# Kernel tuning notes

Hardware: AMD Instinct MI355X
Metric: run time of the kernel (lower is better)

## Reference

```python
import jax, jax.numpy as jnp
import numpy as np

K = 20  # neighbors


def knn_idx(x, k):
    # x: [B, C, N]; returns indices of k nearest neighbors (incl. self): [B, N, k]
    xx = jnp.sum(x * x, axis=1)                          # [B, N]
    inner = jnp.einsum('bcn,bcm->bnm', x, x)             # [B, N, N]
    pd = 2.0 * inner - xx[:, :, None] - xx[:, None, :]   # -squared distance
    _, idx = jax.lax.top_k(pd, k)                        # [B, N, k]
    return idx


def graph_feature(x, k):
    # x: [B, C, N] -> edge features [B, 2C, N, k]
    idx = knn_idx(x, k)                                  # [B, N, k]
    xt = jnp.swapaxes(x, 1, 2)                           # [B, N, C]
    nbr = jax.vmap(lambda f, i: f[i])(xt, idx)           # [B, N, k, C]
    ctr = xt[:, :, None, :]                              # [B, N, 1, C]
    feat = jnp.concatenate(
        [nbr - ctr, jnp.broadcast_to(ctr, nbr.shape)], axis=-1)  # [B, N, k, 2C]
    return jnp.transpose(feat, (0, 3, 1, 2))             # [B, 2C, N, k]


def blk2(x, w, s, t):
    # 1x1 Conv2d (no bias) + folded BN + LeakyReLU(0.2); x: [B, C, N, k]
    y = jnp.einsum('oc,bcnk->bonk', w, x)
    y = y * s[None, :, None, None] + t[None, :, None, None]
    return jax.nn.leaky_relu(y, 0.2)


def blk1(x, w, s, t):
    # 1x1 Conv1d (no bias) + folded BN + LeakyReLU(0.2); x: [B, C, N]
    y = jnp.einsum('oc,bcn->bon', w, x)
    y = y * s[None, :, None] + t[None, :, None]
    return jax.nn.leaky_relu(y, 0.2)


def setup_inputs() -> dict:
    key = jax.random.key(0)
    ks = jax.random.split(key, 32)
    inp = {'x': jax.random.normal(ks[0], (16, 2, 2048), jnp.float32)}
    wdims = [(64, 4), (64, 64), (64, 128), (64, 64), (64, 128),
             (1024, 192), (512, 1216), (256, 512), (1, 256)]
    for i, (o, c) in enumerate(wdims):
        inp[f'w{i+1}'] = jax.random.normal(ks[1 + i], (o, c), jnp.float32) * np.float32((2.0 / c) ** 0.5)
    bdims = [64, 64, 64, 64, 64, 1024, 512, 256]
    for i, d in enumerate(bdims):
        inp[f's{i+1}'] = jax.random.uniform(ks[10 + i], (d,), jnp.float32, 0.5, 1.5)
        inp[f't{i+1}'] = jax.random.normal(ks[18 + i], (d,), jnp.float32) * 0.1
    return inp


def reference(x, w1, w2, w3, w4, w5, w6, w7, w8, w9,
              s1, s2, s3, s4, s5, s6, s7, s8,
              t1, t2, t3, t4, t5, t6, t7, t8):
    B, _, N = x.shape
    h = graph_feature(x, K)                 # [B, 4, N, k]
    h = blk2(h, w1, s1, t1)
    h = blk2(h, w2, s2, t2)
    x1 = jnp.max(h, axis=-1)                # [B, 64, N]
    h = graph_feature(x1, K)                # [B, 128, N, k]
    h = blk2(h, w3, s3, t3)
    h = blk2(h, w4, s4, t4)
    x2 = jnp.max(h, axis=-1)                # [B, 64, N]
    h = graph_feature(x2, K)                # [B, 128, N, k]
    h = blk2(h, w5, s5, t5)
    x3 = jnp.max(h, axis=-1)                # [B, 64, N]
    cat = jnp.concatenate([x1, x2, x3], axis=1)   # [B, 192, N]
    e = blk1(cat, w6, s6, t6)               # [B, 1024, N]
    g = jnp.max(e, axis=-1, keepdims=True)  # global max [B, 1024, 1]
    g = jnp.broadcast_to(g, (B, g.shape[1], N))
    h = jnp.concatenate([g, x1, x2, x3], axis=1)  # [B, 1216, N]
    h = blk1(h, w7, s7, t7)
    h = blk1(h, w8, s8, t8)                 # dropout = identity (eval)
    y = jnp.einsum('oc,bcn->bon', w9, h)    # [B, 1, N]
    return jax.nn.sigmoid(y.reshape(B, -1))
```

## Files before the change

kernel.cpp:

```cpp
#include <hip/hip_runtime.h>
#include <math.h>

#define KNNK 20
#define BEFORE(v1, g1, v2, g2) (((v1) > (v2)) || ((v1) == (v2) && (g1) < (g2)))

typedef unsigned short u16;
typedef unsigned int u32;
typedef __attribute__((ext_vector_type(8))) short short8v;
typedef __attribute__((ext_vector_type(4))) float f32x4;

__device__ __forceinline__ float lrelu(float v) { return v >= 0.f ? v : 0.2f * v; }

__device__ __forceinline__ u16 f2bf(float v) {
    u32 u = __float_as_uint(v);
    u += 0x7fffu + ((u >> 16) & 1u);
    return (u16)(u >> 16);
}
__device__ __forceinline__ float bf2f(u16 h) { return __uint_as_float(((u32)h) << 16); }

__global__ __launch_bounds__(256) void xx_kernel(const float* __restrict__ f, long bstride, int C,
                                                 float* __restrict__ xx) {
    int i = blockIdx.x * 256 + threadIdx.x;
    int b = i >> 11, n = i & 2047;
    const float* fb = f + (long)b * bstride;
    float s = 0.f;
    for (int c = 0; c < C; ++c) { float v = fb[c * 2048 + n]; s = fmaf(v, v, s); }
    xx[i] = s;
}

__global__ __launch_bounds__(512, 4) void knn_kernel(const float* __restrict__ f, long bstride, int C,
                                                     const float* __restrict__ xx, int* __restrict__ idx_out) {
    __shared__ __align__(16) float lds[8 * 2048];
    int b = blockIdx.y;
    int n0 = blockIdx.x * 8;
    int t = threadIdx.x;
    const float* fb = f + (long)b * bstride;

    for (int e = t; e < C * 8; e += 512) {
        int c = e >> 3, j = e & 7;
        lds[e] = fb[c * 2048 + n0 + j];
    }
    __syncthreads();

    float acc[8][4];
#pragma unroll
    for (int i = 0; i < 8; ++i)
#pragma unroll
        for (int j = 0; j < 4; ++j) acc[i][j] = 0.f;
    int m0 = t * 4;
    for (int c = 0; c < C; ++c) {
        float4 b4 = *(const float4*)(fb + c * 2048 + m0);
        float bv[4] = {b4.x, b4.y, b4.z, b4.w};
        float4 a0 = *(const float4*)(lds + c * 8);
        float4 a1 = *(const float4*)(lds + c * 8 + 4);
        float av[8] = {a0.x, a0.y, a0.z, a0.w, a1.x, a1.y, a1.z, a1.w};
#pragma unroll
        for (int i = 0; i < 8; ++i)
#pragma unroll
            for (int j = 0; j < 4; ++j) acc[i][j] = fmaf(av[i], bv[j], acc[i][j]);
    }
    float xn[8];
#pragma unroll
    for (int i = 0; i < 8; ++i) xn[i] = xx[b * 2048 + n0 + i];
    float4 xm4 = *(const float4*)(xx + b * 2048 + m0);
    float xm[4] = {xm4.x, xm4.y, xm4.z, xm4.w};

    __syncthreads();
#pragma unroll
    for (int i = 0; i < 8; ++i) {
        float4 o;
        o.x = (2.f * acc[i][0] - xn[i]) - xm[0];
        o.y = (2.f * acc[i][1] - xn[i]) - xm[1];
        o.z = (2.f * acc[i][2] - xn[i]) - xm[2];
        o.w = (2.f * acc[i][3] - xn[i]) - xm[3];
        *(float4*)(lds + i * 2048 + m0) = o;
    }
    __syncthreads();

    int wave = t >> 6, lane = t & 63;
    const float* srow = lds + wave * 2048;
    float v[32];
#pragma unroll
    for (int j = 0; j < 32; ++j) v[j] = srow[lane + 64 * j];

    float b1 = -INFINITY, b2 = -INFINITY, b3 = -INFINITY;
    int j1 = 0, j2 = 0, j3 = 0;
#pragma unroll
    for (int j = 0; j < 32; ++j) {
        float vv = v[j];
        bool c1 = vv > b1;
        bool c2 = vv > b2;
        bool c3 = vv > b3;
        b3 = c2 ? b2 : (c3 ? vv : b3);
        j3 = c2 ? j2 : (c3 ? j : j3);
        b2 = c1 ? b1 : (c2 ? vv : b2);
        j2 = c1 ? j1 : (c2 ? j : j2);
        b1 = c1 ? vv : b1;
        j1 = c1 ? j : j1;
    }

    float av = b1, bv = b2;
    int ag = lane + (j1 << 6), bg = lane + (j2 << 6);
#pragma unroll
    for (int size = 2; size <= 128; size <<= 1) {
#pragma unroll
        for (int stride = size >> 1; stride >= 1; stride >>= 1) {
            if (stride == 64) {
                bool keep = BEFORE(av, ag, bv, bg);
                float tv = keep ? av : bv;
                int tg = keep ? ag : bg;
                bv = keep ? bv : av; bg = keep ? bg : ag;
                av = tv; ag = tg;
            } else {
                float oav = __shfl_xor(av, stride), obv = __shfl_xor(bv, stride);
                int oag = __shfl_xor(ag, stride), obg = __shfl_xor(bg, stride);
                bool low = (lane & stride) == 0;
                bool ascA = (lane & size) == 0;
                bool ascB = (((64 + lane) & size) == 0);
                bool fA = BEFORE(av, ag, oav, oag);
                bool fB = BEFORE(bv, bg, obv, obg);
                bool tA = (low == ascA) ? fA : !fA;
                bool tB = (low == ascB) ? fB : !fB;
                av = tA ? av : oav; ag = tA ? ag : oag;
                bv = tB ? bv : obv; bg = tB ? bg : obg;
            }
        }
    }
    float wv19 = __shfl(av, 19);
    int wg19 = __shfl(ag, 19);
    unsigned used = (1u << j1) | (1u << j2) | (1u << j3);
    float pv = b3;
    int pg = lane + (j3 << 6);
    while (__any(BEFORE(pv, pg, wv19, wg19))) {
        unsigned long long act = __ballot(BEFORE(pv, pg, wv19, wg19));
        int L = __ffsll(act) - 1;
        float cv = __shfl(pv, L);
        int cg2 = __shfl(pg, L);
        unsigned long long cfb = __ballot(lane < 20 && BEFORE(cv, cg2, av, ag));
        int p = 20 - __popcll(cfb);
        float upv = __shfl_up(av, 1);
        int upg = __shfl_up(ag, 1);
        if (lane < 20) {
            if (lane > p) { av = upv; ag = upg; }
            else if (lane == p) { av = cv; ag = cg2; }
        }
        if (lane == L) {
            float nb = -INFINITY;
            int nj = 0;
#pragma unroll
            for (int j = 0; j < 32; ++j) {
                float vvv = ((used >> j) & 1u) ? -INFINITY : v[j];
                if (vvv > nb) { nb = vvv; nj = j; }
            }
            used |= 1u << nj;
            pv = nb;
            pg = lane + (nj << 6);
        }
        wv19 = __shfl(av, 19);
        wg19 = __shfl(ag, 19);
    }
    int* orow = idx_out + ((long)b * 2048 + n0 + wave) * KNNK;
    if (lane < KNNK) orow[lane] = ag;
}

__global__ __launch_bounds__(256) void pq_kernel(const float* __restrict__ f, long bstride, int C,
                                                 const float* __restrict__ W, float* __restrict__ P,
                                                 float* __restrict__ Q) {
    __shared__ __align__(16) float wa[64 * 64];
    __shared__ __align__(16) float wq[64 * 64];
    __shared__ __align__(16) float X[64 * 64];
    int b = blockIdx.y, n0 = blockIdx.x * 64, t = threadIdx.x;
    const float* fb = f + (long)b * bstride;
    for (int e = t; e < C * 64; e += 256) {
        int k = e >> 6, c = e & 63;
        float a = W[c * 2 * C + k];
        float bv = W[c * 2 * C + C + k];
        wa[k * 64 + c] = a;
        wq[k * 64 + c] = bv - a;
    }
    for (int e = t; e < C * 64; e += 256) {
        int k = e >> 6, j = e & 63;
        X[e] = fb[k * 2048 + n0 + j];
    }
    __syncthreads();
    int cg = t >> 4, ng = t & 15;
    float accP[4][4] = {}, accQ[4][4] = {};
    for (int k = 0; k < C; ++k) {
        float4 a4 = *(const float4*)(wa + k * 64 + cg * 4);
        float4 q4 = *(const float4*)(wq + k * 64 + cg * 4);
        float4 x4 = *(const float4*)(X + k * 64 + ng * 4);
        float av[4] = {a4.x, a4.y, a4.z, a4.w};
        float qv[4] = {q4.x, q4.y, q4.z, q4.w};
        float xv[4] = {x4.x, x4.y, x4.z, x4.w};
#pragma unroll
        for (int i = 0; i < 4; ++i)
#pragma unroll
            for (int j = 0; j < 4; ++j) {
                accP[i][j] = fmaf(av[i], xv[j], accP[i][j]);
                accQ[i][j] = fmaf(qv[i], xv[j], accQ[i][j]);
            }
    }
#pragma unroll
    for (int j = 0; j < 4; ++j) {
        long n = n0 + ng * 4 + j;
        float4 pv = {accP[0][j], accP[1][j], accP[2][j], accP[3][j]};
        float4 qv = {accQ[0][j], accQ[1][j], accQ[2][j], accQ[3][j]};
        *(float4*)(P + ((long)b * 2048 + n) * 64 + cg * 4) = pv;
        *(float4*)(Q + ((long)b * 2048 + n) * 64 + cg * 4) = qv;
    }
}

__global__ __launch_bounds__(256) void edge2_kernel(
    const float* __restrict__ P, const float* __restrict__ Q, const int* __restrict__ idx,
    const float* __restrict__ W2, const float* __restrict__ sa, const float* __restrict__ ta,
    const float* __restrict__ sb, const float* __restrict__ tb, float* __restrict__ out, int cofs) {
    __shared__ __align__(16) float h1[64 * 164];
    __shared__ __align__(16) float w2l[64 * 64];
    __shared__ int idxl[160];
    int b = blockIdx.y, n0 = blockIdx.x * 8, t = threadIdx.x;
    if (t < 160) idxl[t] = idx[((long)b * 2048 + n0) * KNNK + t];
    for (int e = t; e < 4096; e += 256) { int co = e >> 6, ci = e & 63; w2l[ci * 64 + co] = W2[e]; }
    __syncthreads();
    for (int it = t; it < 2560; it += 256) {
        int col = it % 160, cg = it / 160;
        int p = col / 20;
        int j = idxl[col];
        int n = n0 + p;
        float4 pv = *(const float4*)(P + ((long)b * 2048 + j) * 64 + cg * 4);
        float4 qv = *(const float4*)(Q + ((long)b * 2048 + n) * 64 + cg * 4);
        float4 sv = *(const float4*)(sa + cg * 4);
        float4 tv = *(const float4*)(ta + cg * 4);
        h1[(cg * 4 + 0) * 164 + col] = lrelu(fmaf(sv.x, pv.x + qv.x, tv.x));
        h1[(cg * 4 + 1) * 164 + col] = lrelu(fmaf(sv.y, pv.y + qv.y, tv.y));
        h1[(cg * 4 + 2) * 164 + col] = lrelu(fmaf(sv.z, pv.z + qv.z, tv.z));
        h1[(cg * 4 + 3) * 164 + col] = lrelu(fmaf(sv.w, pv.w + qv.w, tv.w));
    }
    __syncthreads();
    int p = t & 7, co2 = t >> 3, c0 = co2 * 2;
    float acc0[20], acc1[20];
#pragma unroll
    for (int q = 0; q < 20; ++q) { acc0[q] = 0.f; acc1[q] = 0.f; }
#pragma unroll 4
    for (int k = 0; k < 64; ++k) {
        float2 w = *(const float2*)(w2l + k * 64 + c0);
        const float* hr = h1 + k * 164 + p * 20;
#pragma unroll
        for (int q = 0; q < 5; ++q) {
            float4 h4 = *(const float4*)(hr + q * 4);
            acc0[q * 4 + 0] = fmaf(w.x, h4.x, acc0[q * 4 + 0]);
            acc0[q * 4 + 1] = fmaf(w.x, h4.y, acc0[q * 4 + 1]);
            acc0[q * 4 + 2] = fmaf(w.x, h4.z, acc0[q * 4 + 2]);
            acc0[q * 4 + 3] = fmaf(w.x, h4.w, acc0[q * 4 + 3]);
            acc1[q * 4 + 0] = fmaf(w.y, h4.x, acc1[q * 4 + 0]);
            acc1[q * 4 + 1] = fmaf(w.y, h4.y, acc1[q * 4 + 1]);
            acc1[q * 4 + 2] = fmaf(w.y, h4.z, acc1[q * 4 + 2]);
            acc1[q * 4 + 3] = fmaf(w.y, h4.w, acc1[q * 4 + 3]);
        }
    }
    float s0 = sb[c0], t0v = tb[c0], s1 = sb[c0 + 1], t1v = tb[c0 + 1];
    float m0 = -INFINITY, m1 = -INFINITY;
#pragma unroll
    for (int q = 0; q < 20; ++q) {
        m0 = fmaxf(m0, lrelu(fmaf(s0, acc0[q], t0v)));
        m1 = fmaxf(m1, lrelu(fmaf(s1, acc1[q], t1v)));
    }
    out[(long)b * (192 * 2048) + (long)(cofs + c0) * 2048 + n0 + p] = m0;
    out[(long)b * (192 * 2048) + (long)(cofs + c0 + 1) * 2048 + n0 + p] = m1;
}

__global__ __launch_bounds__(256) void edge1_kernel(const float* __restrict__ P, const float* __restrict__ Q,
                                                    const int* __restrict__ idx, const float* __restrict__ s,
                                                    const float* __restrict__ tt, float* __restrict__ out,
                                                    int cofs) {
    __shared__ int idxl[80];
    int b = blockIdx.y, n0 = blockIdx.x * 4, t = threadIdx.x;
    int c = t & 63, p = t >> 6;
    if (t < 80) idxl[t] = idx[((long)b * 2048 + n0) * KNNK + t];
    __syncthreads();
    float qv = Q[((long)b * 2048 + n0 + p) * 64 + c];
    float sc = s[c], tc = tt[c];
    float m = -INFINITY;
    for (int kk = 0; kk < KNNK; ++kk) {
        int j = idxl[p * KNNK + kk];
        float v = P[((long)b * 2048 + j) * 64 + c];
        m = fmaxf(m, lrelu(fmaf(sc, v + qv, tc)));
    }
    out[(long)b * (192 * 2048) + (long)(cofs + c) * 2048 + n0 + p] = m;
}

__global__ __launch_bounds__(256) void gemm_kernel(
    const float* __restrict__ W, int ldw, int Kdim, const float* __restrict__ X, long xbstride,
    const float* __restrict__ s, const float* __restrict__ tvec, const float* __restrict__ bias, int M,
    float* __restrict__ out, long obstride, float* __restrict__ maxout) {
    __shared__ __align__(16) float wl[32 * 68];
    __shared__ __align__(16) float xl[32 * 132];
    int b = blockIdx.z, ct = blockIdx.x * 64, nt = blockIdx.y * 128, t = threadIdx.x;
    const float* Xb = X + (long)b * xbstride;
    int cg = t >> 4, ng = t & 15;
    float acc[4][8];
#pragma unroll
    for (int i = 0; i < 4; ++i)
#pragma unroll
        for (int j = 0; j < 8; ++j) acc[i][j] = 0.f;
    for (int k0 = 0; k0 < Kdim; k0 += 32) {
        __syncthreads();
        for (int e = t; e < 2048; e += 256) {
            int c = e >> 5, k = e & 31;
            wl[k * 68 + c] = W[(long)(ct + c) * ldw + k0 + k];
        }
        for (int e = t; e < 4096; e += 256) {
            int k = e >> 7, j = e & 127;
            xl[k * 132 + j] = Xb[(long)(k0 + k) * 2048 + nt + j];
        }
        __syncthreads();
#pragma unroll 8
        for (int k = 0; k < 32; ++k) {
            float4 w4 = *(const float4*)(wl + k * 68 + cg * 4);
            float4 xa = *(const float4*)(xl + k * 132 + ng * 4);
            float4 xb = *(const float4*)(xl + k * 132 + 64 + ng * 4);
            float wv[4] = {w4.x, w4.y, w4.z, w4.w};
            float xv[8] = {xa.x, xa.y, xa.z, xa.w, xb.x, xb.y, xb.z, xb.w};
#pragma unroll
            for (int i = 0; i < 4; ++i)
#pragma unroll
                for (int j = 0; j < 8; ++j) acc[i][j] = fmaf(wv[i], xv[j], acc[i][j]);
        }
    }
    if (maxout) {
        __syncthreads();
        float* scr = xl;
#pragma unroll
        for (int i = 0; i < 4; ++i) {
            int c = ct + cg * 4 + i;
            float sv = s[c], tv = tvec[c];
            float m = -INFINITY;
#pragma unroll
            for (int j = 0; j < 8; ++j) m = fmaxf(m, lrelu(fmaf(sv, acc[i][j], tv)));
            scr[(cg * 4 + i) * 16 + ng] = m;
        }
        __syncthreads();
        if (t < 64) {
            float m = scr[t * 16];
            for (int j = 1; j < 16; ++j) m = fmaxf(m, scr[t * 16 + j]);
            maxout[((long)b * M + ct + t) * 16 + blockIdx.y] = m;
        }
    } else {
#pragma unroll
        for (int i = 0; i < 4; ++i) {
            int c = ct + cg * 4 + i;
            float bv = bias ? bias[b * M + c] : 0.f;
            float sv = s[c], tv = tvec[c];
            float4 o0, o1;
            o0.x = lrelu(fmaf(sv, acc[i][0] + bv, tv));
            o0.y = lrelu(fmaf(sv, acc[i][1] + bv, tv));
            o0.z = lrelu(fmaf(sv, acc[i][2] + bv, tv));
            o0.w = lrelu(fmaf(sv, acc[i][3] + bv, tv));
            o1.x = lrelu(fmaf(sv, acc[i][4] + bv, tv));
            o1.y = lrelu(fmaf(sv, acc[i][5] + bv, tv));
            o1.z = lrelu(fmaf(sv, acc[i][6] + bv, tv));
            o1.w = lrelu(fmaf(sv, acc[i][7] + bv, tv));
            float* op = out + (long)b * obstride + (long)c * 2048 + nt + ng * 4;
            *(float4*)op = o0;
            *(float4*)(op + 64) = o1;
        }
    }
}

__global__ __launch_bounds__(256) void splitw_kernel(const float* __restrict__ W, int ldw, int koff, int K,
                                                     long total, u16* __restrict__ hi, u16* __restrict__ lo) {
    long i = (long)blockIdx.x * 256 + threadIdx.x;
    if (i >= total) return;
    long m = i / K, k = i - m * K;
    float v = W[m * ldw + koff + k];
    u16 h = f2bf(v);
    hi[i] = h;
    lo[i] = f2bf(v - bf2f(h));
}

__global__ __launch_bounds__(256) void splitx_kernel(const float* __restrict__ cat, u16* __restrict__ hi,
                                                     u16* __restrict__ lo) {
    __shared__ float lds[32][65];
    int b = blockIdx.y;
    int kt = blockIdx.x % 6, nt = blockIdx.x / 6;
    int k0 = kt * 32, n0 = nt * 64;
    int t = threadIdx.x;
#pragma unroll
    for (int i = 0; i < 8; ++i) {
        int e = t + i * 256;
        int k = e >> 6, n = e & 63;
        lds[k][n] = cat[(long)b * (192 * 2048) + (long)(k0 + k) * 2048 + n0 + n];
    }
    __syncthreads();
    int n = t >> 2, kq = t & 3;
    u16 hv[8], lv[8];
#pragma unroll
    for (int i = 0; i < 8; ++i) {
        float v = lds[kq * 8 + i][n];
        u16 h = f2bf(v);
        hv[i] = h;
        lv[i] = f2bf(v - bf2f(h));
    }
    long off = ((long)b * 2048 + n0 + n) * 192 + k0 + kq * 8;
    uint4 uh, ul;
    uh.x = (u32)hv[0] | ((u32)hv[1] << 16); uh.y = (u32)hv[2] | ((u32)hv[3] << 16);
    uh.z = (u32)hv[4] | ((u32)hv[5] << 16); uh.w = (u32)hv[6] | ((u32)hv[7] << 16);
    ul.x = (u32)lv[0] | ((u32)lv[1] << 16); ul.y = (u32)lv[2] | ((u32)lv[3] << 16);
    ul.z = (u32)lv[4] | ((u32)lv[5] << 16); ul.w = (u32)lv[6] | ((u32)lv[7] << 16);
    *(uint4*)(hi + off) = uh;
    *(uint4*)(lo + off) = ul;
}

template <int MT, int NT, bool MAXOUT>
__global__ __launch_bounds__(256, 2) void gemm_mfma(
    const u16* __restrict__ Whi, const u16* __restrict__ Wlo, const u16* __restrict__ Xhi,
    const u16* __restrict__ Xlo, int K, int M, const float* __restrict__ s,
    const float* __restrict__ tvec, const float* __restrict__ bias, float* __restrict__ outf,
    long obstride, u16* __restrict__ ohi, u16* __restrict__ olo, int oK, float* __restrict__ maxout) {
    constexpr int BM = MT * 32, BN = NT * 32;
    __shared__ __align__(16) u16 Ah[BM * 32], Al[BM * 32], Bh[BN * 32], Bl[BN * 32];
    __shared__ float scr[MAXOUT ? BM * 2 : 1];

    int b = blockIdx.z;
    int m0 = blockIdx.x * BM;
    int n0 = blockIdx.y * BN;
    int t = threadIdx.x;
    int wave = t >> 6, lane = t & 63;
    int wm = (wave >> 1) * (MT * 16);
    int wn = (wave & 1) * (NT * 16);
    const int l15 = lane & 15, lq = lane >> 4;
    const int kcs = lq ^ ((l15 >> 1) & 3);

    const u16* Xbh = Xhi + (long)b * 2048 * K;
    const u16* Xbl = Xlo + (long)b * 2048 * K;

    f32x4 zero4 = {0.f, 0.f, 0.f, 0.f};
    f32x4 acc[MT][NT];
#pragma unroll
    for (int i = 0; i < MT; ++i)
#pragma unroll
        for (int j = 0; j < NT; ++j) acc[i][j] = zero4;

    for (int k0 = 0; k0 < K; k0 += 32) {
        __syncthreads();
#pragma unroll
        for (int u = t; u < BM * 4; u += 256) {
            int row = u >> 2, kc = (u & 3) ^ ((row >> 1) & 3);
            long ga = (long)(m0 + row) * K + k0 + kc * 8;
            *(uint4*)(Ah + u * 8) = *(const uint4*)(Whi + ga);
            *(uint4*)(Al + u * 8) = *(const uint4*)(Wlo + ga);
        }
#pragma unroll
        for (int u = t; u < BN * 4; u += 256) {
            int row = u >> 2, kc = (u & 3) ^ ((row >> 1) & 3);
            long ga = (long)(n0 + row) * K + k0 + kc * 8;
            *(uint4*)(Bh + u * 8) = *(const uint4*)(Xbh + ga);
            *(uint4*)(Bl + u * 8) = *(const uint4*)(Xbl + ga);
        }
        __syncthreads();
        short8v a_h[MT], a_l[MT], b_h[NT], b_l[NT];
#pragma unroll
        for (int i = 0; i < MT; ++i) {
            int u = (wm + i * 16 + l15) * 4 + kcs;
            a_h[i] = *(const short8v*)(Ah + u * 8);
            a_l[i] = *(const short8v*)(Al + u * 8);
        }
#pragma unroll
        for (int j = 0; j < NT; ++j) {
            int u = (wn + j * 16 + l15) * 4 + kcs;
            b_h[j] = *(const short8v*)(Bh + u * 8);
            b_l[j] = *(const short8v*)(Bl + u * 8);
        }
#pragma unroll
        for (int i = 0; i < MT; ++i)
#pragma unroll
            for (int j = 0; j < NT; ++j) {
                acc[i][j] = __builtin_amdgcn_mfma_f32_16x16x32_bf16(a_h[i], b_h[j], acc[i][j], 0, 0, 0);
                acc[i][j] = __builtin_amdgcn_mfma_f32_16x16x32_bf16(a_h[i], b_l[j], acc[i][j], 0, 0, 0);
                acc[i][j] = __builtin_amdgcn_mfma_f32_16x16x32_bf16(a_l[i], b_h[j], acc[i][j], 0, 0, 0);
            }
    }

    if constexpr (MAXOUT) {
#pragma unroll
        for (int i = 0; i < MT; ++i)
#pragma unroll
            for (int r = 0; r < 4; ++r) {
                int ml = wm + i * 16 + lq * 4 + r;
                int c = m0 + ml;
                float sv = s[c], tv = tvec[c];
                float mx = -INFINITY;
#pragma unroll
                for (int j = 0; j < NT; ++j) mx = fmaxf(mx, lrelu(fmaf(sv, acc[i][j][r], tv)));
                mx = fmaxf(mx, __shfl_xor(mx, 1));
                mx = fmaxf(mx, __shfl_xor(mx, 2));
                mx = fmaxf(mx, __shfl_xor(mx, 4));
                mx = fmaxf(mx, __shfl_xor(mx, 8));
                if (l15 == 0) scr[ml * 2 + (wave & 1)] = mx;
            }
        __syncthreads();
        if (t < BM) maxout[((long)b * M + m0 + t) * 16 + blockIdx.y] = fmaxf(scr[t * 2], scr[t * 2 + 1]);
    } else if (outf) {
#pragma unroll
        for (int i = 0; i < MT; ++i)
#pragma unroll
            for (int r = 0; r < 4; ++r) {
                int c = m0 + wm + i * 16 + lq * 4 + r;
                float sv = s[c], tv = tvec[c];
                float bv = bias ? bias[b * M + c] : 0.f;
                float* op = outf + (long)b * obstride + (long)c * 2048 + n0 + wn;
#pragma unroll
                for (int j = 0; j < NT; ++j) op[j * 16 + l15] = lrelu(fmaf(sv, acc[i][j][r] + bv, tv));
            }
    } else {
#pragma unroll
        for (int i = 0; i < MT; ++i) {
            float sv[4], tv[4], bv[4];
#pragma unroll
            for (int r = 0; r < 4; ++r) {
                int c = m0 + wm + i * 16 + lq * 4 + r;
                sv[r] = s[c];
                tv[r] = tvec[c];
                bv[r] = bias ? bias[b * M + c] : 0.f;
            }
#pragma unroll
            for (int j = 0; j < NT; ++j) {
                long nb = ((long)b * 2048 + n0 + wn + j * 16 + l15) * oK + m0 + wm + i * 16 + lq * 4;
                ushort4 uh, ul;
                float v0 = lrelu(fmaf(sv[0], acc[i][j][0] + bv[0], tv[0]));
                float v1 = lrelu(fmaf(sv[1], acc[i][j][1] + bv[1], tv[1]));
                float v2 = lrelu(fmaf(sv[2], acc[i][j][2] + bv[2], tv[2]));
                float v3 = lrelu(fmaf(sv[3], acc[i][j][3] + bv[3], tv[3]));
                u16 h0 = f2bf(v0), h1 = f2bf(v1), h2 = f2bf(v2), h3 = f2bf(v3);
                uh.x = h0; uh.y = h1; uh.z = h2; uh.w = h3;
                ul.x = f2bf(v0 - bf2f(h0));
                ul.y = f2bf(v1 - bf2f(h1));
                ul.z = f2bf(v2 - bf2f(h2));
                ul.w = f2bf(v3 - bf2f(h3));
                *(ushort4*)(ohi + nb) = uh;
                *(ushort4*)(olo + nb) = ul;
            }
        }
    }
}

__global__ __launch_bounds__(256) void gmax_final(const float* __restrict__ ep, float* __restrict__ g) {
    int i = blockIdx.x * 256 + threadIdx.x;
    float m = ep[i * 16];
    for (int j = 1; j < 16; ++j) m = fmaxf(m, ep[i * 16 + j]);
    g[i] = m;
}

__global__ __launch_bounds__(64) void bias7_kernel(const float* __restrict__ w7, const float* __restrict__ g,
                                                   float* __restrict__ bias7) {
    int o = blockIdx.x;
    int b = o >> 9, co = o & 511;
    int lane = threadIdx.x;
    float acc = 0.f;
    for (int j = lane; j < 1024; j += 64) acc = fmaf(w7[(long)co * 1216 + j], g[b * 1024 + j], acc);
#pragma unroll
    for (int off = 32; off >= 1; off >>= 1) acc += __shfl_xor(acc, off);
    if (lane == 0) bias7[o] = acc;
}

__global__ __launch_bounds__(256) void w9_kernel(const float* __restrict__ w9, const float* __restrict__ h8,
                                                 float* __restrict__ out) {
    int i = blockIdx.x * 256 + threadIdx.x;
    int b = i >> 11, n = i & 2047;
    const float* hb = h8 + (long)b * 256 * 2048 + n;
    float acc = 0.f;
    for (int c = 0; c < 256; ++c) acc = fmaf(w9[c], hb[c * 2048], acc);
    out[i] = 1.f / (1.f + expf(-acc));
}

extern "C" void kernel_launch(void* const* d_in, const int* in_sizes, int n_in,
                              void* d_out, int out_size, void* d_ws, size_t ws_size,
                              hipStream_t stream) {
    (void)in_sizes; (void)n_in; (void)out_size;
    const float* x  = (const float*)d_in[0];
    const float* w1 = (const float*)d_in[1];
    const float* w2 = (const float*)d_in[2];
    const float* w3 = (const float*)d_in[3];
    const float* w4 = (const float*)d_in[4];
    const float* w5 = (const float*)d_in[5];
    const float* w6 = (const float*)d_in[6];
    const float* w7 = (const float*)d_in[7];
    const float* w8 = (const float*)d_in[8];
    const float* w9 = (const float*)d_in[9];
    const float* s1 = (const float*)d_in[10]; const float* t1 = (const float*)d_in[11];
    const float* s2 = (const float*)d_in[12]; const float* t2 = (const float*)d_in[13];
    const float* s3 = (const float*)d_in[14]; const float* t3 = (const float*)d_in[15];
    const float* s4 = (const float*)d_in[16]; const float* t4 = (const float*)d_in[17];
    const float* s5 = (const float*)d_in[18]; const float* t5 = (const float*)d_in[19];
    const float* s6 = (const float*)d_in[20]; const float* t6 = (const float*)d_in[21];
    const float* s7 = (const float*)d_in[22]; const float* t7 = (const float*)d_in[23];
    const float* s8 = (const float*)d_in[24]; const float* t8 = (const float*)d_in[25];

    float* cat = (float*)d_ws;
    float* xxb = cat + (long)6291456;
    int* idxb = (int*)(xxb + 32768);
    float* ep = (float*)(idxb + 655360);
    float* g  = ep + 262144;
    float* b7 = g + 16384;
    float* h8 = b7 + 8192;
    float* P  = h8 + 8388608;
    float* Q  = P + 2097152;
    u16* h7hi = (u16*)(Q + 2097152);
    u16* h7lo = h7hi + 16777216;
    u16* cathi = h7lo + 16777216;
    u16* catlo = cathi + 6291456;
    u16* w6h = catlo + 6291456;
    u16* w6l = w6h + 196608;
    u16* w7h = w6l + 196608;
    u16* w7l = w7h + 98304;
    u16* w8h = w7l + 98304;
    u16* w8l = w8h + 131072;
    const size_t NEED = 173375488;

    dim3 blk(256);
    dim3 blk512(512);
    long catstride = 192 * 2048;

    xx_kernel<<<128, blk, 0, stream>>>(x, 2 * 2048, 2, xxb);
    knn_kernel<<<dim3(256, 16), blk512, 0, stream>>>(x, 2 * 2048, 2, xxb, idxb);
    pq_kernel<<<dim3(32, 16), blk, 0, stream>>>(x, 2 * 2048, 2, w1, P, Q);
    edge2_kernel<<<dim3(256, 16), blk, 0, stream>>>(P, Q, idxb, w2, s1, t1, s2, t2, cat, 0);
    xx_kernel<<<128, blk, 0, stream>>>(cat, catstride, 64, xxb);
    knn_kernel<<<dim3(256, 16), blk512, 0, stream>>>(cat, catstride, 64, xxb, idxb);
    pq_kernel<<<dim3(32, 16), blk, 0, stream>>>(cat, catstride, 64, w3, P, Q);
    edge2_kernel<<<dim3(256, 16), blk, 0, stream>>>(P, Q, idxb, w4, s3, t3, s4, t4, cat, 64);
    xx_kernel<<<128, blk, 0, stream>>>(cat + 64 * 2048, catstride, 64, xxb);
    knn_kernel<<<dim3(256, 16), blk512, 0, stream>>>(cat + 64 * 2048, catstride, 64, xxb, idxb);
    pq_kernel<<<dim3(32, 16), blk, 0, stream>>>(cat + 64 * 2048, catstride, 64, w5, P, Q);
    edge1_kernel<<<dim3(512, 16), blk, 0, stream>>>(P, Q, idxb, s5, t5, cat, 128);

    if (ws_size >= NEED) {
        splitw_kernel<<<768, blk, 0, stream>>>(w6, 192, 0, 192, 196608, w6h, w6l);
        splitw_kernel<<<384, blk, 0, stream>>>(w7, 1216, 1024, 192, 98304, w7h, w7l);
        splitw_kernel<<<512, blk, 0, stream>>>(w8, 512, 0, 512, 131072, w8h, w8l);
        splitx_kernel<<<dim3(192, 16), blk, 0, stream>>>(cat, cathi, catlo);
        gemm_mfma<4, 4, true><<<dim3(8, 16, 16), blk, 0, stream>>>(
            w6h, w6l, cathi, catlo, 192, 1024, s6, t6, nullptr, nullptr, 0, nullptr, nullptr, 0, ep);
        gmax_final<<<64, blk, 0, stream>>>(ep, g);
        bias7_kernel<<<dim3(16 * 512), dim3(64), 0, stream>>>(w7, g, b7);
        gemm_mfma<4, 4, false><<<dim3(4, 16, 16), blk, 0, stream>>>(
            w7h, w7l, cathi, catlo, 192, 512, s7, t7, b7, nullptr, 0, h7hi, h7lo, 512, nullptr);
        gemm_mfma<2, 4, false><<<dim3(4, 16, 16), blk, 0, stream>>>(
            w8h, w8l, h7hi, h7lo, 512, 256, s8, t8, nullptr, h8, (long)256 * 2048, nullptr, nullptr, 0,
            nullptr);
        w9_kernel<<<128, blk, 0, stream>>>(w9, h8, (float*)d_out);
    } else {
        float* h7f = (float*)h7hi;
        gemm_kernel<<<dim3(16, 16, 16), blk, 0, stream>>>(w6, 192, 192, cat, catstride, s6, t6, nullptr,
                                                          1024, nullptr, 0, ep);
        gmax_final<<<64, blk, 0, stream>>>(ep, g);
        bias7_kernel<<<dim3(16 * 512), dim3(64), 0, stream>>>(w7, g, b7);
        gemm_kernel<<<dim3(8, 16, 16), blk, 0, stream>>>(w7 + 1024, 1216, 192, cat, catstride, s7, t7, b7,
                                                         512, h7f, (long)512 * 2048, nullptr);
        gemm_kernel<<<dim3(4, 16, 16), blk, 0, stream>>>(w8, 512, 512, h7f, (long)512 * 2048, s8, t8,
                                                         nullptr, 256, h8, (long)256 * 2048, nullptr);
        w9_kernel<<<128, blk, 0, stream>>>(w9, h8, (float*)d_out);
    }
}
```

Measured before the change: 1.098 ms.

## Compute 64-channel kNN distances with split-bf16 MFMA instead of FP32 FMA

```diff
diff --git a/kernel.cpp b/kernel.cpp
--- a/kernel.cpp
+++ b/kernel.cpp
@@ -28,57 +28,7 @@
     xx[i] = s;
 }
 
-__global__ __launch_bounds__(512, 4) void knn_kernel(const float* __restrict__ f, long bstride, int C,
-                                                     const float* __restrict__ xx, int* __restrict__ idx_out) {
-    __shared__ __align__(16) float lds[8 * 2048];
-    int b = blockIdx.y;
-    int n0 = blockIdx.x * 8;
-    int t = threadIdx.x;
-    const float* fb = f + (long)b * bstride;
-
-    for (int e = t; e < C * 8; e += 512) {
-        int c = e >> 3, j = e & 7;
-        lds[e] = fb[c * 2048 + n0 + j];
-    }
-    __syncthreads();
-
-    float acc[8][4];
-#pragma unroll
-    for (int i = 0; i < 8; ++i)
-#pragma unroll
-        for (int j = 0; j < 4; ++j) acc[i][j] = 0.f;
-    int m0 = t * 4;
-    for (int c = 0; c < C; ++c) {
-        float4 b4 = *(const float4*)(fb + c * 2048 + m0);
-        float bv[4] = {b4.x, b4.y, b4.z, b4.w};
-        float4 a0 = *(const float4*)(lds + c * 8);
-        float4 a1 = *(const float4*)(lds + c * 8 + 4);
-        float av[8] = {a0.x, a0.y, a0.z, a0.w, a1.x, a1.y, a1.z, a1.w};
-#pragma unroll
-        for (int i = 0; i < 8; ++i)
-#pragma unroll
-            for (int j = 0; j < 4; ++j) acc[i][j] = fmaf(av[i], bv[j], acc[i][j]);
-    }
-    float xn[8];
-#pragma unroll
-    for (int i = 0; i < 8; ++i) xn[i] = xx[b * 2048 + n0 + i];
-    float4 xm4 = *(const float4*)(xx + b * 2048 + m0);
-    float xm[4] = {xm4.x, xm4.y, xm4.z, xm4.w};
-
-    __syncthreads();
-#pragma unroll
-    for (int i = 0; i < 8; ++i) {
-        float4 o;
-        o.x = (2.f * acc[i][0] - xn[i]) - xm[0];
-        o.y = (2.f * acc[i][1] - xn[i]) - xm[1];
-        o.z = (2.f * acc[i][2] - xn[i]) - xm[2];
-        o.w = (2.f * acc[i][3] - xn[i]) - xm[3];
-        *(float4*)(lds + i * 2048 + m0) = o;
-    }
-    __syncthreads();
-
-    int wave = t >> 6, lane = t & 63;
-    const float* srow = lds + wave * 2048;
+__device__ __forceinline__ void topk_row(const float* __restrict__ srow, int lane, int* __restrict__ orow) {
     float v[32];
 #pragma unroll
     for (int j = 0; j < 32; ++j) v[j] = srow[lane + 64 * j];
@@ -159,8 +109,166 @@
         wv19 = __shfl(av, 19);
         wg19 = __shfl(ag, 19);
     }
-    int* orow = idx_out + ((long)b * 2048 + n0 + wave) * KNNK;
     if (lane < KNNK) orow[lane] = ag;
+}
+
+__global__ __launch_bounds__(512, 4) void knn_kernel(const float* __restrict__ f, long bstride, int C,
+                                                     const float* __restrict__ xx, int* __restrict__ idx_out) {
+    __shared__ __align__(16) float lds[8 * 2048];
+    int b = blockIdx.y;
+    int n0 = blockIdx.x * 8;
+    int t = threadIdx.x;
+    const float* fb = f + (long)b * bstride;
+
+    for (int e = t; e < C * 8; e += 512) {
+        int c = e >> 3, j = e & 7;
+        lds[e] = fb[c * 2048 + n0 + j];
+    }
+    __syncthreads();
+
+    float acc[8][4];
+#pragma unroll
+    for (int i = 0; i < 8; ++i)
+#pragma unroll
+        for (int j = 0; j < 4; ++j) acc[i][j] = 0.f;
+    int m0 = t * 4;
+    for (int c = 0; c < C; ++c) {
+        float4 b4 = *(const float4*)(fb + c * 2048 + m0);
+        float bv[4] = {b4.x, b4.y, b4.z, b4.w};
+        float4 a0 = *(const float4*)(lds + c * 8);
+        float4 a1 = *(const float4*)(lds + c * 8 + 4);
+        float av[8] = {a0.x, a0.y, a0.z, a0.w, a1.x, a1.y, a1.z, a1.w};
+#pragma unroll
+        for (int i = 0; i < 8; ++i)
+#pragma unroll
+            for (int j = 0; j < 4; ++j) acc[i][j] = fmaf(av[i], bv[j], acc[i][j]);
+    }
+    float xn[8];
+#pragma unroll
+    for (int i = 0; i < 8; ++i) xn[i] = xx[b * 2048 + n0 + i];
+    float4 xm4 = *(const float4*)(xx + b * 2048 + m0);
+    float xm[4] = {xm4.x, xm4.y, xm4.z, xm4.w};
+
+    __syncthreads();
+#pragma unroll
+    for (int i = 0; i < 8; ++i) {
+        float4 o;
+        o.x = (2.f * acc[i][0] - xn[i]) - xm[0];
+        o.y = (2.f * acc[i][1] - xn[i]) - xm[1];
+        o.z = (2.f * acc[i][2] - xn[i]) - xm[2];
+        o.w = (2.f * acc[i][3] - xn[i]) - xm[3];
+        *(float4*)(lds + i * 2048 + m0) = o;
+    }
+    __syncthreads();
+
+    int wave = t >> 6, lane = t & 63;
+    topk_row(lds + wave * 2048, lane, idx_out + ((long)b * 2048 + n0 + wave) * KNNK);
+}
+
+__global__ __launch_bounds__(256) void split3t_kernel(const float* __restrict__ src, long bstride,
+                                                      u16* __restrict__ oh, u16* __restrict__ om,
+                                                      u16* __restrict__ ol) {
+    __shared__ float lds[32][65];
+    int b = blockIdx.y;
+    int kt = blockIdx.x & 1, nt = blockIdx.x >> 1;
+    int k0 = kt * 32, n0 = nt * 64, t = threadIdx.x;
+#pragma unroll
+    for (int i = 0; i < 8; ++i) {
+        int e = t + i * 256;
+        int k = e >> 6, n = e & 63;
+        lds[k][n] = src[(long)b * bstride + (long)(k0 + k) * 2048 + n0 + n];
+    }
+    __syncthreads();
+    int n = t >> 2, kq = t & 3;
+    u16 hv[8], mv[8], lv[8];
+#pragma unroll
+    for (int i = 0; i < 8; ++i) {
+        float v = lds[kq * 8 + i][n];
+        u16 h = f2bf(v);
+        float r1 = v - bf2f(h);
+        u16 m = f2bf(r1);
+        float r2 = r1 - bf2f(m);
+        hv[i] = h; mv[i] = m; lv[i] = f2bf(r2);
+    }
+    long off = ((long)b * 2048 + n0 + n) * 64 + k0 + kq * 8;
+    uint4 uh, um, ul;
+    uh.x = (u32)hv[0] | ((u32)hv[1] << 16); uh.y = (u32)hv[2] | ((u32)hv[3] << 16);
+    uh.z = (u32)hv[4] | ((u32)hv[5] << 16); uh.w = (u32)hv[6] | ((u32)hv[7] << 16);
+    um.x = (u32)mv[0] | ((u32)mv[1] << 16); um.y = (u32)mv[2] | ((u32)mv[3] << 16);
+    um.z = (u32)mv[4] | ((u32)mv[5] << 16); um.w = (u32)mv[6] | ((u32)mv[7] << 16);
+    ul.x = (u32)lv[0] | ((u32)lv[1] << 16); ul.y = (u32)lv[2] | ((u32)lv[3] << 16);
+    ul.z = (u32)lv[4] | ((u32)lv[5] << 16); ul.w = (u32)lv[6] | ((u32)lv[7] << 16);
+    *(uint4*)(oh + off) = uh;
+    *(uint4*)(om + off) = um;
+    *(uint4*)(ol + off) = ul;
+}
+
+__global__ __launch_bounds__(512) void knn_mfma_kernel(const u16* __restrict__ Sh, const u16* __restrict__ Sm,
+                                                       const u16* __restrict__ Sl, const float* __restrict__ xx,
+                                                       int* __restrict__ idx_out) {
+    __shared__ __align__(16) float pd[8 * 2048];
+    int b = blockIdx.y, n0 = blockIdx.x * 16, t = threadIdx.x;
+    int wave = t >> 6, lane = t & 63, l15 = lane & 15, lq = lane >> 4;
+    const u16* bh_ = Sh + (long)b * 2048 * 64;
+    const u16* bm_ = Sm + (long)b * 2048 * 64;
+    const u16* bl_ = Sl + (long)b * 2048 * 64;
+
+    long ab = (long)(n0 + l15) * 64 + lq * 8;
+    short8v ah0 = *(const short8v*)(bh_ + ab), ah1 = *(const short8v*)(bh_ + ab + 32);
+    short8v am0 = *(const short8v*)(bm_ + ab), am1 = *(const short8v*)(bm_ + ab + 32);
+    short8v al0 = *(const short8v*)(bl_ + ab), al1 = *(const short8v*)(bl_ + ab + 32);
+
+    float4 xn4 = *(const float4*)(xx + b * 2048 + n0 + lq * 4);
+    int jbase = wave * 256;
+    f32x4 acc[16];
+#pragma unroll
+    for (int ct = 0; ct < 16; ++ct) {
+        long bb = (long)(jbase + ct * 16 + l15) * 64 + lq * 8;
+        short8v bh0 = *(const short8v*)(bh_ + bb), bh1 = *(const short8v*)(bh_ + bb + 32);
+        short8v bm0 = *(const short8v*)(bm_ + bb), bm1 = *(const short8v*)(bm_ + bb + 32);
+        short8v bl0 = *(const short8v*)(bl_ + bb), bl1 = *(const short8v*)(bl_ + bb + 32);
+        f32x4 p = {0.f, 0.f, 0.f, 0.f}, q = {0.f, 0.f, 0.f, 0.f};
+        p = __builtin_amdgcn_mfma_f32_16x16x32_bf16(ah0, bh0, p, 0, 0, 0);
+        q = __builtin_amdgcn_mfma_f32_16x16x32_bf16(ah0, bm0, q, 0, 0, 0);
+        p = __builtin_amdgcn_mfma_f32_16x16x32_bf16(am0, bh0, p, 0, 0, 0);
+        q = __builtin_amdgcn_mfma_f32_16x16x32_bf16(am0, bm0, q, 0, 0, 0);
+        p = __builtin_amdgcn_mfma_f32_16x16x32_bf16(ah0, bl0, p, 0, 0, 0);
+        q = __builtin_amdgcn_mfma_f32_16x16x32_bf16(al0, bh0, q, 0, 0, 0);
+        p = __builtin_amdgcn_mfma_f32_16x16x32_bf16(ah1, bh1, p, 0, 0, 0);
+        q = __builtin_amdgcn_mfma_f32_16x16x32_bf16(ah1, bm1, q, 0, 0, 0);
+        p = __builtin_amdgcn_mfma_f32_16x16x32_bf16(am1, bh1, p, 0, 0, 0);
+        q = __builtin_amdgcn_mfma_f32_16x16x32_bf16(am1, bm1, q, 0, 0, 0);
+        p = __builtin_amdgcn_mfma_f32_16x16x32_bf16(ah1, bl1, p, 0, 0, 0);
+        q = __builtin_amdgcn_mfma_f32_16x16x32_bf16(al1, bh1, q, 0, 0, 0);
+        float xmc = xx[b * 2048 + jbase + ct * 16 + l15];
+        f32x4 r = p + q;
+        acc[ct][0] = 2.f * r[0] - xn4.x - xmc;
+        acc[ct][1] = 2.f * r[1] - xn4.y - xmc;
+        acc[ct][2] = 2.f * r[2] - xn4.z - xmc;
+        acc[ct][3] = 2.f * r[3] - xn4.w - xmc;
+    }
+
+    if (lq < 2) {
+#pragma unroll
+        for (int ct = 0; ct < 16; ++ct) {
+            int col = jbase + ct * 16 + l15;
+#pragma unroll
+            for (int r = 0; r < 4; ++r) pd[(lq * 4 + r) * 2048 + col] = acc[ct][r];
+        }
+    }
+    __syncthreads();
+    topk_row(pd + wave * 2048, lane, idx_out + ((long)b * 2048 + n0 + wave) * KNNK);
+    __syncthreads();
+    if (lq >= 2) {
+#pragma unroll
+        for (int ct = 0; ct < 16; ++ct) {
+            int col = jbase + ct * 16 + l15;
+#pragma unroll
+            for (int r = 0; r < 4; ++r) pd[((lq - 2) * 4 + r) * 2048 + col] = acc[ct][r];
+        }
+    }
+    __syncthreads();
+    topk_row(pd + wave * 2048, lane, idx_out + ((long)b * 2048 + n0 + 8 + wave) * KNNK);
 }
 
 __global__ __launch_bounds__(256) void pq_kernel(const float* __restrict__ f, long bstride, int C,
@@ -615,6 +723,11 @@
     u16* w8h = w7l + 98304;
     u16* w8l = w8h + 131072;
     const size_t NEED = 173375488;
+    bool big = ws_size >= NEED;
+
+    u16* Sh = h7hi;
+    u16* Sm = h7hi + 2097152;
+    u16* Sl = h7hi + 4194304;
 
     dim3 blk(256);
     dim3 blk512(512);
@@ -625,15 +738,25 @@
     pq_kernel<<<dim3(32, 16), blk, 0, stream>>>(x, 2 * 2048, 2, w1, P, Q);
     edge2_kernel<<<dim3(256, 16), blk, 0, stream>>>(P, Q, idxb, w2, s1, t1, s2, t2, cat, 0);
     xx_kernel<<<128, blk, 0, stream>>>(cat, catstride, 64, xxb);
-    knn_kernel<<<dim3(256, 16), blk512, 0, stream>>>(cat, catstride, 64, xxb, idxb);
+    if (big) {
+        split3t_kernel<<<dim3(64, 16), blk, 0, stream>>>(cat, catstride, Sh, Sm, Sl);
+        knn_mfma_kernel<<<dim3(128, 16), blk512, 0, stream>>>(Sh, Sm, Sl, xxb, idxb);
+    } else {
+        knn_kernel<<<dim3(256, 16), blk512, 0, stream>>>(cat, catstride, 64, xxb, idxb);
+    }
     pq_kernel<<<dim3(32, 16), blk, 0, stream>>>(cat, catstride, 64, w3, P, Q);
     edge2_kernel<<<dim3(256, 16), blk, 0, stream>>>(P, Q, idxb, w4, s3, t3, s4, t4, cat, 64);
     xx_kernel<<<128, blk, 0, stream>>>(cat + 64 * 2048, catstride, 64, xxb);
-    knn_kernel<<<dim3(256, 16), blk512, 0, stream>>>(cat + 64 * 2048, catstride, 64, xxb, idxb);
+    if (big) {
+        split3t_kernel<<<dim3(64, 16), blk, 0, stream>>>(cat + 64 * 2048, catstride, Sh, Sm, Sl);
+        knn_mfma_kernel<<<dim3(128, 16), blk512, 0, stream>>>(Sh, Sm, Sl, xxb, idxb);
+    } else {
+        knn_kernel<<<dim3(256, 16), blk512, 0, stream>>>(cat + 64 * 2048, catstride, 64, xxb, idxb);
+    }
     pq_kernel<<<dim3(32, 16), blk, 0, stream>>>(cat + 64 * 2048, catstride, 64, w5, P, Q);
     edge1_kernel<<<dim3(512, 16), blk, 0, stream>>>(P, Q, idxb, s5, t5, cat, 128);
 
-    if (ws_size >= NEED) {
+    if (big) {
         splitw_kernel<<<768, blk, 0, stream>>>(w6, 192, 0, 192, 196608, w6h, w6l);
         splitw_kernel<<<384, blk, 0, stream>>>(w7, 1216, 1024, 192, 98304, w7h, w7l);
         splitw_kernel<<<512, blk, 0, stream>>>(w8, 512, 0, 512, 131072, w8h, w8l);
```

Measured after the change: 1.374 ms. 1.25x slower.
